# Performance work log

Hardware: AMD Instinct MI355X
Metric: run time of the kernel (lower is better)

## Reference

```python
import jax, jax.numpy as jnp
import numpy as np


def setup_inputs() -> dict:
    key = jax.random.key(0)
    k1, k2, k3, k4 = jax.random.split(key, 4)
    B, n, f, k = 32768, 512, 30, 40
    X = jax.random.normal(k1, (B, n), dtype=jnp.float32)
    w1 = jax.random.normal(k2, (n, 1), dtype=jnp.float32) * 0.01
    b = jnp.zeros((1,), dtype=jnp.float32)
    v = jax.random.normal(k3, (n, f, k), dtype=jnp.float32) * 0.01
    feature2field = jax.random.randint(k4, (n,), 0, f, dtype=jnp.int32)
    return {"X": X, "w1": w1, "b": b, "v": v, "feature2field": feature2field}


def reference(X, w1, b, v, feature2field):
    # linear terms: [B]
    linear = (X @ w1).reshape(-1) + b[0]
    n = v.shape[0]
    # A[i, j] = v[i, feature2field[j]]  -> [n, n, k]
    A = v[:, feature2field, :]
    # pair coefficient C[i, j] = sum_k v[i, field[j], k] * v[j, field[i], k]
    C = jnp.einsum('ijk,jik->ij', A, A)
    # strict upper triangle matches the i<j loop in the original
    Cm = C * jnp.triu(jnp.ones((n, n), dtype=C.dtype), k=1)
    # interaction[b] = sum_{i<j} C[i,j] * X[b,i] * X[b,j]
    inter = jnp.einsum('bi,ij,bj->b', X, Cm, X)
    logits = linear + inter
    return jax.nn.sigmoid(logits)
```

## Files before the change

kernel.cpp:

```cpp
#include <hip/hip_runtime.h>
#include <hip/hip_bf16.h>
#include <math.h>


#define N_FEAT 512
#define FK 1200
#define KDIM 40
#define B_ROWS 32768
#define BM 64
#define BK 64

typedef __attribute__((ext_vector_type(8))) short short8;
typedef __attribute__((ext_vector_type(4))) float f32x4;

__device__ __forceinline__ unsigned short bf16_rne(float f) {
    union { float f; unsigned int u; } c; c.f = f;
    unsigned int u = c.u;
    u += 0x7fffu + ((u >> 16) & 1u);
    return (unsigned short)(u >> 16);
}

__device__ __forceinline__ float bf16_to_f(unsigned short h) {
    union { unsigned int u; float f; } c;
    c.u = ((unsigned int)h) << 16;
    return c.f;
}

__device__ __forceinline__ void async_copy16(const void* g, void* l) {
    __builtin_amdgcn_global_load_lds(
        (const __attribute__((address_space(1))) void*)g,
        (__attribute__((address_space(3))) void*)l,
        16, 0, 0);
}

#define FENCE() asm volatile("" ::: "memory")

__global__ __launch_bounds__(256) void build_w16(const float* __restrict__ v,
                                                 const int* __restrict__ f2f,
                                                 unsigned short* __restrict__ W16) {
    const int j = blockIdx.x * 256 + threadIdx.x;
    const int i = blockIdx.y;
    const int fi = f2f[i];
    const int fj = f2f[j];
    const float4* a = (const float4*)(v + (size_t)i * FK + (size_t)fj * KDIM);
    const float4* c = (const float4*)(v + (size_t)j * FK + (size_t)fi * KDIM);
    float acc = 0.f;
#pragma unroll
    for (int q = 0; q < KDIM / 4; ++q) {
        float4 av = a[q], cv = c[q];
        acc = fmaf(av.x, cv.x, acc);
        acc = fmaf(av.y, cv.y, acc);
        acc = fmaf(av.z, cv.z, acc);
        acc = fmaf(av.w, cv.w, acc);
    }
    W16[(size_t)i * N_FEAT + j] = (i == j) ? (unsigned short)0 : bf16_rne(0.5f * acc);
}

__global__ __launch_bounds__(512, 2) void ffm_fused(const float* __restrict__ X,
                                                    const unsigned short* __restrict__ W16,
                                                    const float* __restrict__ w1,
                                                    const float* __restrict__ bvec,
                                                    float* __restrict__ out) {
    __shared__ __align__(16) unsigned short As[BM * N_FEAT];
    __shared__ __align__(16) unsigned short Bs[2][128 * BK];
    __shared__ float part[4 * BM];

    const int tid  = threadIdx.x;
    const int lane = tid & 63;
    const int wave = tid >> 6;
    const int wm = wave & 1;
    const int wn = wave >> 1;
    const int quad = lane >> 4;
    const int l16  = lane & 15;
    const int aswz = l16 & 7;

    const size_t row0 = (size_t)blockIdx.x * BM;

    const int srow = lane >> 3;
    const int scol = (((lane & 7) ^ srow) << 3);

    float w1v[4][2];
#pragma unroll
    for (int cb = 0; cb < 4; ++cb)
#pragma unroll
        for (int ni = 0; ni < 2; ++ni)
            w1v[cb][ni] = w1[cb * 128 + wn * 32 + ni * 16 + l16];
    const float bias = bvec[0];

    auto stage = [&](int s) {
        const int col0 = (s >> 3) * 128;
        const int k0   = (s & 7) * 64;
        unsigned short* dst = (unsigned short*)Bs[s & 1];
#pragma unroll
        for (int c = 0; c < 2; ++c) {
            const int chunk = wave * 2 + c;
            const int r = chunk * 8 + srow;
            async_copy16(W16 + (size_t)(col0 + r) * N_FEAT + k0 + scol,
                         dst + chunk * 512);
        }
    };

    stage(0);
    {
        const float4* X4 = (const float4*)(X + row0 * N_FEAT);
#pragma unroll
        for (int u = 0; u < 8; ++u) {
            const int g  = u * 512 + tid;
            const int r  = g >> 6;
            const int cc = g & 63;
            float4 f0 = X4[r * 128 + cc * 2];
            float4 f1 = X4[r * 128 + cc * 2 + 1];
            union { unsigned short us[8]; short8 v; } pk;
            pk.us[0] = bf16_rne(f0.x);
            pk.us[1] = bf16_rne(f0.y);
            pk.us[2] = bf16_rne(f0.z);
            pk.us[3] = bf16_rne(f0.w);
            pk.us[4] = bf16_rne(f1.x);
            pk.us[5] = bf16_rne(f1.y);
            pk.us[6] = bf16_rne(f1.z);
            pk.us[7] = bf16_rne(f1.w);
            *(short8*)(As + r * N_FEAT + ((cc ^ (r & 7)) << 3)) = pk.v;
        }
    }
    asm volatile("s_waitcnt lgkmcnt(0)" ::: "memory");
    __builtin_amdgcn_s_barrier();
    FENCE();

    float rs[2][4];
#pragma unroll
    for (int mi = 0; mi < 2; ++mi)
#pragma unroll
        for (int reg = 0; reg < 4; ++reg) rs[mi][reg] = 0.f;

    f32x4 acc[2][2];
#pragma unroll
    for (int mi = 0; mi < 2; ++mi)
#pragma unroll
        for (int ni = 0; ni < 2; ++ni)
            acc[mi][ni] = (f32x4){0.f, 0.f, 0.f, 0.f};

#pragma unroll
    for (int cb = 0; cb < 4; ++cb) {
        const int col0 = cb * 128;
#pragma unroll
        for (int t = 0; t < 8; ++t) {
            const int s = cb * 8 + t;
            if (s < 31) {
                stage(s + 1);
                asm volatile("s_waitcnt vmcnt(2)" ::: "memory");
            } else {
                asm volatile("s_waitcnt vmcnt(0)" ::: "memory");
            }
            __builtin_amdgcn_s_barrier();
            FENCE();

            const unsigned short* bs = (const unsigned short*)Bs[s & 1];
            const int k0 = t * 64;
#pragma unroll
            for (int kk = 0; kk < 2; ++kk) {
                short8 a[2], b[2];
                const int kc = (k0 >> 3) + kk * 4 + quad;
#pragma unroll
                for (int mi = 0; mi < 2; ++mi) {
                    const int ar = wm * 32 + mi * 16 + l16;
                    a[mi] = *(const short8*)(As + ar * N_FEAT + ((kc ^ aswz) << 3));
                }
                const int swc = ((kk * 4 + quad) ^ aswz) << 3;
#pragma unroll
                for (int ni = 0; ni < 2; ++ni) {
                    const int br = wn * 32 + ni * 16 + l16;
                    b[ni] = *(const short8*)(bs + br * BK + swc);
                }
#pragma unroll
                for (int mi = 0; mi < 2; ++mi)
#pragma unroll
                    for (int ni = 0; ni < 2; ++ni)
                        acc[mi][ni] = __builtin_amdgcn_mfma_f32_16x16x32_bf16(
                            a[mi], b[ni], acc[mi][ni], 0, 0, 0);
            }

            FENCE();
            __builtin_amdgcn_s_barrier();
            FENCE();
        }

#pragma unroll
        for (int mi = 0; mi < 2; ++mi) {
#pragma unroll
            for (int ni = 0; ni < 2; ++ni) {
                const int gc = col0 + wn * 32 + ni * 16 + l16;
#pragma unroll
                for (int reg = 0; reg < 4; ++reg) {
                    const int row = wm * 32 + mi * 16 + quad * 4 + reg;
                    const int adr = row * N_FEAT + ((((gc >> 3) ^ (row & 7)) << 3) | (gc & 7));
                    const float xf = bf16_to_f(As[adr]);
                    rs[mi][reg] = fmaf(xf, acc[mi][ni][reg] + w1v[cb][ni], rs[mi][reg]);
                }
                acc[mi][ni] = (f32x4){0.f, 0.f, 0.f, 0.f};
            }
        }
    }

#pragma unroll
    for (int mi = 0; mi < 2; ++mi)
#pragma unroll
        for (int reg = 0; reg < 4; ++reg) {
            float r = rs[mi][reg];
#pragma unroll
            for (int off = 1; off < 16; off <<= 1)
                r += __shfl_xor(r, off, 16);
            if (l16 == 0)
                part[wn * BM + wm * 32 + mi * 16 + quad * 4 + reg] = r;
        }
    __syncthreads();

    if (tid < BM) {
        const float t = part[tid] + part[BM + tid] + part[2 * BM + tid] +
                        part[3 * BM + tid] + bias;
        out[row0 + tid] = 1.0f / (1.0f + expf(-t));
    }
}

extern "C" void kernel_launch(void* const* d_in, const int* in_sizes, int n_in,
                              void* d_out, int out_size, void* d_ws, size_t ws_size,
                              hipStream_t stream) {
    const float* X   = (const float*)d_in[0];
    const float* w1  = (const float*)d_in[1];
    const float* b   = (const float*)d_in[2];
    const float* v   = (const float*)d_in[3];
    const int*   f2f = (const int*)d_in[4];
    float* out = (float*)d_out;

    unsigned short* W16 = (unsigned short*)d_ws;

    build_w16<<<dim3(2, N_FEAT), 256, 0, stream>>>(v, f2f, W16);
    ffm_fused<<<B_ROWS / BM, 512, 0, stream>>>(X, W16, w1, b, out);
}
```

Before: 141.7 us.

## Keep A fragments in registers, double B k-tile, stage v in LDS for W build

```diff
diff --git a/kernel.cpp b/kernel.cpp
--- a/kernel.cpp
+++ b/kernel.cpp
@@ -8,7 +8,7 @@
 #define KDIM 40
 #define B_ROWS 32768
 #define BM 64
-#define BK 64
+#define BK2 128
 
 typedef __attribute__((ext_vector_type(8))) short short8;
 typedef __attribute__((ext_vector_type(4))) float f32x4;
@@ -38,12 +38,26 @@
 __global__ __launch_bounds__(256) void build_w16(const float* __restrict__ v,
                                                  const int* __restrict__ f2f,
                                                  unsigned short* __restrict__ W16) {
-    const int j = blockIdx.x * 256 + threadIdx.x;
-    const int i = blockIdx.y;
-    const int fi = f2f[i];
+    __shared__ float a_lds[FK];
+    __shared__ float c_lds[256 * 44];
+
+    const int i   = blockIdx.y;
+    const int j0  = blockIdx.x * 256;
+    const int tid = threadIdx.x;
+    const int fi  = f2f[i];
+
+    for (int q = tid; q < FK; q += 256) a_lds[q] = v[(size_t)i * FK + q];
+    for (int q = tid; q < 2560; q += 256) {
+        const int jl = q / 10, c4 = q % 10;
+        *(float4*)&c_lds[jl * 44 + c4 * 4] =
+            *(const float4*)&v[(size_t)(j0 + jl) * FK + fi * KDIM + c4 * 4];
+    }
+    __syncthreads();
+
+    const int j  = j0 + tid;
     const int fj = f2f[j];
-    const float4* a = (const float4*)(v + (size_t)i * FK + (size_t)fj * KDIM);
-    const float4* c = (const float4*)(v + (size_t)j * FK + (size_t)fi * KDIM);
+    const float4* a = (const float4*)&a_lds[fj * KDIM];
+    const float4* c = (const float4*)&c_lds[tid * 44];
     float acc = 0.f;
 #pragma unroll
     for (int q = 0; q < KDIM / 4; ++q) {
@@ -62,7 +76,7 @@
                                                     const float* __restrict__ bvec,
                                                     float* __restrict__ out) {
     __shared__ __align__(16) unsigned short As[BM * N_FEAT];
-    __shared__ __align__(16) unsigned short Bs[2][128 * BK];
+    __shared__ __align__(16) unsigned short Bs[2][128 * BK2];
     __shared__ float part[4 * BM];
 
     const int tid  = threadIdx.x;
@@ -76,9 +90,6 @@
 
     const size_t row0 = (size_t)blockIdx.x * BM;
 
-    const int srow = lane >> 3;
-    const int scol = (((lane & 7) ^ srow) << 3);
-
     float w1v[4][2];
 #pragma unroll
     for (int cb = 0; cb < 4; ++cb)
@@ -88,15 +99,14 @@
     const float bias = bvec[0];
 
     auto stage = [&](int s) {
-        const int col0 = (s >> 3) * 128;
-        const int k0   = (s & 7) * 64;
+        const int col0 = (s >> 2) * 128;
+        const int k0   = (s & 3) * BK2;
         unsigned short* dst = (unsigned short*)Bs[s & 1];
 #pragma unroll
-        for (int c = 0; c < 2; ++c) {
-            const int chunk = wave * 2 + c;
-            const int r = chunk * 8 + srow;
-            async_copy16(W16 + (size_t)(col0 + r) * N_FEAT + k0 + scol,
-                         dst + chunk * 512);
+        for (int i = 0; i < 4; ++i) {
+            const int r = wave * 16 + i * 4 + quad;
+            async_copy16(W16 + (size_t)(col0 + r) * N_FEAT + k0 + ((l16 ^ (r & 7)) << 3),
+                         dst + r * BK2 + l16 * 8);
         }
     };
 
@@ -126,6 +136,15 @@
     __builtin_amdgcn_s_barrier();
     FENCE();
 
+    short8 areg[2][16];
+#pragma unroll
+    for (int ka = 0; ka < 16; ++ka)
+#pragma unroll
+        for (int mi = 0; mi < 2; ++mi) {
+            const int ar = wm * 32 + mi * 16 + l16;
+            areg[mi][ka] = *(const short8*)(As + ar * N_FEAT + (((ka * 4 + quad) ^ aswz) << 3));
+        }
+
     float rs[2][4];
 #pragma unroll
     for (int mi = 0; mi < 2; ++mi)
@@ -143,11 +162,11 @@
     for (int cb = 0; cb < 4; ++cb) {
         const int col0 = cb * 128;
 #pragma unroll
-        for (int t = 0; t < 8; ++t) {
-            const int s = cb * 8 + t;
-            if (s < 31) {
+        for (int t = 0; t < 4; ++t) {
+            const int s = cb * 4 + t;
+            if (s < 15) {
                 stage(s + 1);
-                asm volatile("s_waitcnt vmcnt(2)" ::: "memory");
+                asm volatile("s_waitcnt vmcnt(4)" ::: "memory");
             } else {
                 asm volatile("s_waitcnt vmcnt(0)" ::: "memory");
             }
@@ -155,29 +174,25 @@
             FENCE();
 
             const unsigned short* bs = (const unsigned short*)Bs[s & 1];
-            const int k0 = t * 64;
-#pragma unroll
-            for (int kk = 0; kk < 2; ++kk) {
-                short8 a[2], b[2];
-                const int kc = (k0 >> 3) + kk * 4 + quad;
-#pragma unroll
-                for (int mi = 0; mi < 2; ++mi) {
-                    const int ar = wm * 32 + mi * 16 + l16;
-                    a[mi] = *(const short8*)(As + ar * N_FEAT + ((kc ^ aswz) << 3));
-                }
+            __builtin_amdgcn_s_setprio(1);
+#pragma unroll
+            for (int kk = 0; kk < 4; ++kk) {
+                const int ka = t * 4 + kk;
+                short8 b[2];
                 const int swc = ((kk * 4 + quad) ^ aswz) << 3;
 #pragma unroll
                 for (int ni = 0; ni < 2; ++ni) {
                     const int br = wn * 32 + ni * 16 + l16;
-                    b[ni] = *(const short8*)(bs + br * BK + swc);
+                    b[ni] = *(const short8*)(bs + br * BK2 + swc);
                 }
 #pragma unroll
                 for (int mi = 0; mi < 2; ++mi)
 #pragma unroll
                     for (int ni = 0; ni < 2; ++ni)
                         acc[mi][ni] = __builtin_amdgcn_mfma_f32_16x16x32_bf16(
-                            a[mi], b[ni], acc[mi][ni], 0, 0, 0);
+                            areg[mi][ka], b[ni], acc[mi][ni], 0, 0, 0);
             }
+            __builtin_amdgcn_s_setprio(0);
 
             FENCE();
             __builtin_amdgcn_s_barrier();
```

After: 155.2 us. 1.09x slower.
